# Optimization experiments

Measured on AMD Instinct MI355X. Metric: run time of the kernel, lower is better.

## Reference

```python
import jax, jax.numpy as jnp
import numpy as np

B, N, X, H = 128, 512, 128, 256  # batch, seq len, in features, hidden

_PARAM_SHAPES = [
    ("fg_w_c", (H,)), ("fg_w_h", (H, H)), ("fg_w_x", (H, X)), ("fg_b", (H,)),
    ("ig_w_c", (H,)), ("ig_w_h", (H, H)), ("ig_w_x", (H, X)), ("ig_b", (H,)),
    ("in_w_h", (H, H)), ("in_w_x", (H, X)), ("in_b", (H,)),
    ("og_w_cn", (H,)), ("og_w_h", (H, H)), ("og_w_x", (H, X)), ("og_b", (H,)), ("og_w_t", (H,)),
    ("tg1_w_x", (H, X)), ("tg1_w_t", (H,)), ("tg1_b", (H,)),
    ("tg2_w_x", (H, X)), ("tg2_w_t", (H,)), ("tg2_b", (H,)),
]


def setup_inputs() -> dict:
    key = jax.random.key(0)
    ks = jax.random.split(key, 2 + len(_PARAM_SHAPES))
    stdv = 1.0 / np.sqrt(H)  # torch __init__ re-inits all params uniform(-stdv, stdv)
    inp = {
        "x": jax.random.normal(ks[0], (B, N, X), jnp.float32),
        "t": jax.random.uniform(ks[1], (B, N, 1), jnp.float32),  # time intervals >= 0
    }
    for i, (name, shape) in enumerate(_PARAM_SHAPES):
        inp[name] = jax.random.uniform(ks[2 + i], shape, jnp.float32, -stdv, stdv)
    return inp


def reference(x, t,
              fg_w_c, fg_w_h, fg_w_x, fg_b,
              ig_w_c, ig_w_h, ig_w_x, ig_b,
              in_w_h, in_w_x, in_b,
              og_w_cn, og_w_h, og_w_x, og_b, og_w_t,
              tg1_w_x, tg1_w_t, tg1_b,
              tg2_w_x, tg2_w_t, tg2_b):
    # TimeLSTM_v3 with nn_type = NN_TYPE_LSTM_TIME2.
    # torch stores vector params as [H,1] and x_cur as [B,xm,1]; here squeezed to [H] / [B,xm].
    # Precompute all input-dependent (non-recurrent) gate terms over the whole sequence: [B,N,H]
    fg_x = jnp.einsum('bnx,hx->bnh', x, fg_w_x) + fg_b
    ig_x = jnp.einsum('bnx,hx->bnh', x, ig_w_x) + ig_b
    in_x = jnp.einsum('bnx,hx->bnh', x, in_w_x) + in_b
    og_x = jnp.einsum('bnx,hx->bnh', x, og_w_x) + og_w_t * t + og_b
    # Time gates depend only on x and t -> fully precomputable
    tm1 = jax.nn.sigmoid(jnp.einsum('bnx,hx->bnh', x, tg1_w_x) + jnp.tanh(tg1_w_t * t) + tg1_b)
    tm2 = jax.nn.sigmoid(jnp.einsum('bnx,hx->bnh', x, tg2_w_x) + jnp.tanh(tg2_w_t * t) + tg2_b)

    def step(carry, inputs):
        h, cm = carry  # each [B,H]
        fg_xt, ig_xt, in_xt, og_xt, tm1_t, tm2_t = inputs
        ig = jax.nn.sigmoid(ig_w_c * cm + h @ ig_w_h.T + ig_xt)
        fg = jax.nn.sigmoid(fg_w_c * cm + h @ fg_w_h.T + fg_xt)
        inn = jnp.tanh(h @ in_w_h.T + in_xt)
        cm_hat = fg * cm + ig * tm1_t * inn
        cm_new = fg * cm + ig * tm2_t * inn
        og = jax.nn.sigmoid(og_w_cn * cm_hat + h @ og_w_h.T + og_xt)
        h_new = og * jnp.tanh(cm_hat)
        return (h_new, cm_new), None

    seqs = tuple(jnp.moveaxis(a, 1, 0) for a in (fg_x, ig_x, in_x, og_x, tm1, tm2))  # [N,B,H]
    init = (jnp.zeros((x.shape[0], H), x.dtype), jnp.zeros((x.shape[0], H), x.dtype))
    (h, cm), _ = jax.lax.scan(step, init, seqs)
    return h, cm  # h: [B,H] (torch squeezes trailing 1), cm: [B,H]
```

## Files before the change

### kernel.cpp

```cpp
#include <hip/hip_runtime.h>
#include <math.h>

#define BATCH 128
#define SEQN  512
#define XF    128
#define HF    256
#define BC    16
#define HC    8
#define TCH   8
#define NBLK  256
#define NTHR  256
#define NGRP  8
#define GSZ   32

#define OFF_W    0
#define OFF_WX   8192
#define OFF_G    14336
#define OFF_U    20480
#define OFF_SCR  24576
#define OFF_CM   36864
#define OFF_TV   36992
#define OFF_COEF 37120
#define LDS_WORDS 37216
#define LDS_BYTES (LDS_WORDS * 4)

struct Params {
  const float* x;
  const float* t;
  const float* w_h[4];
  const float* w_x[6];
  const float* coef[12];
  float* h_buf;
  unsigned* flags;
  float* out;
};

__device__ __forceinline__ float sigmoidf_(float v) { return 1.0f / (1.0f + __expf(-v)); }

__device__ __forceinline__ void post_arrive(unsigned* flags, int gi, int mi, unsigned step) {
  __syncthreads();
  if (threadIdx.x == 0) {
    __hip_atomic_store(&flags[(gi * GSZ + mi) * 16], step,
                       __ATOMIC_RELAXED, __HIP_MEMORY_SCOPE_AGENT);
  }
}

__device__ __forceinline__ void wait_peers(unsigned* flags, int gi, int mi, unsigned step) {
  if (threadIdx.x < GSZ && threadIdx.x != (unsigned)mi) {
    const unsigned* f = &flags[(gi * GSZ + threadIdx.x) * 16];
    while (__hip_atomic_load(f, __ATOMIC_RELAXED, __HIP_MEMORY_SCOPE_AGENT) < step) {}
  }
  __syncthreads();
}

__global__ __launch_bounds__(NTHR, 1) void timelstm_kernel(Params p) {
  extern __shared__ float sm[];
  const int tid = threadIdx.x;
  const int bid = blockIdx.x;
  const int gi = bid & 7;
  const int mi = bid >> 3;
  const int b0 = gi * BC;
  const int h0 = mi * HC;

  for (int i = tid; i < 4 * 8 * 256; i += NTHR) {
    int g = i >> 11, j = (i >> 8) & 7, k = i & 255;
    sm[OFF_W + k * 32 + j * 4 + g] = p.w_h[g][(h0 + j) * HF + k];
  }
  for (int i = tid; i < 6 * 8 * 128; i += NTHR) {
    int g = i >> 10, j = (i >> 7) & 7, k = i & 127;
    sm[OFF_WX + k * 48 + j * 6 + g] = p.w_x[g][(h0 + j) * XF + k];
  }
  if (tid < 96) sm[OFF_COEF + tid] = p.coef[tid >> 3][h0 + (tid & 7)];
  if (tid < 128) sm[OFF_CM + tid] = 0.0f;
  if (mi == 0) {
    unsigned long long* hbu = (unsigned long long*)p.h_buf;
    for (int i = tid; i < HF * BC / 2; i += NTHR) {
      const int k = i >> 3;
      __hip_atomic_store(&hbu[k * (BATCH / 2) + b0 / 2 + (i & 7)], 0ull,
                         __ATOMIC_RELAXED, __HIP_MEMORY_SCOPE_AGENT);
    }
  }
  unsigned bstep = 1;
  post_arrive(p.flags, gi, mi, bstep);
  wait_peers(p.flags, gi, mi, bstep);
  ++bstep;

  int cur = 0;
  for (int tc0 = 0; tc0 < SEQN; tc0 += TCH) {
    {
      for (int it = 0; it < BC; ++it) {
        const int b = it, t = (tid >> 5) & 7, k0 = (tid & 31) * 4;
        const float4 v = *(const float4*)&p.x[((size_t)(b0 + b) * SEQN + (tc0 + t)) * XF + k0];
        float vb[4] = {v.x, v.y, v.z, v.w};
#pragma unroll
        for (int u = 0; u < 4; ++u) {
          const int k = k0 + u;
          sm[OFF_U + k * 128 + ((((b) << 3) | t) ^ (((k >> 2) & 7) << 2))] = vb[u];
        }
      }
      if (tid < 128)
        sm[OFF_TV + tid] = p.t[(size_t)(b0 + (tid >> 3)) * SEQN + tc0 + (tid & 7)];
    }
    __syncthreads();
    {
      const int gh = tid >> 7, idx = tid & 127;
      const int j = idx >> 4, b = idx & 15;
      float a0[8], a1[8], a2[8];
#pragma unroll
      for (int u = 0; u < 8; ++u) { a0[u] = 0.f; a1[u] = 0.f; a2[u] = 0.f; }
      const int base = b << 3;
#pragma unroll 2
      for (int k = 0; k < XF; ++k) {
        const int xk = ((k >> 2) & 7) << 2;
        const float4 xlo = *(const float4*)&sm[OFF_U + k * 128 + ((base | 0) ^ xk)];
        const float4 xhi = *(const float4*)&sm[OFF_U + k * 128 + ((base | 4) ^ xk)];
        const float* wr = &sm[OFF_WX + k * 48 + j * 6 + gh * 3];
        const float w0 = wr[0], w1 = wr[1], w2 = wr[2];
        const float xs[8] = {xlo.x, xlo.y, xlo.z, xlo.w, xhi.x, xhi.y, xhi.z, xhi.w};
#pragma unroll
        for (int u = 0; u < 8; ++u) {
          a0[u] += w0 * xs[u];
          a1[u] += w1 * xs[u];
          a2[u] += w2 * xs[u];
        }
      }
      if (gh == 0) {
        const float c0 = sm[OFF_COEF + 0 * 8 + j];
        const float c1 = sm[OFF_COEF + 1 * 8 + j];
        const float c2 = sm[OFF_COEF + 2 * 8 + j];
#pragma unroll
        for (int t = 0; t < 8; ++t) {
          sm[OFF_G + t * 768 + 0 * 128 + idx] = a0[t] + c0;
          sm[OFF_G + t * 768 + 1 * 128 + idx] = a1[t] + c1;
          sm[OFF_G + t * 768 + 2 * 128 + idx] = a2[t] + c2;
        }
      } else {
        const float ogb = sm[OFF_COEF + 3 * 8 + j], ogwt = sm[OFF_COEF + 4 * 8 + j];
        const float t1w = sm[OFF_COEF + 5 * 8 + j], t1b = sm[OFF_COEF + 6 * 8 + j];
        const float t2w = sm[OFF_COEF + 7 * 8 + j], t2b = sm[OFF_COEF + 8 * 8 + j];
#pragma unroll
        for (int t = 0; t < 8; ++t) {
          const float tv = sm[OFF_TV + b * 8 + t];
          sm[OFF_G + t * 768 + 3 * 128 + idx] = a0[t] + ogwt * tv + ogb;
          sm[OFF_G + t * 768 + 4 * 128 + idx] = sigmoidf_(a1[t] + tanhf(t1w * tv) + t1b);
          sm[OFF_G + t * 768 + 5 * 128 + idx] = sigmoidf_(a2[t] + tanhf(t2w * tv) + t2b);
        }
      }
    }
    __syncthreads();

    for (int tt = 0; tt < TCH; ++tt) {
      {
        const unsigned long long* hsrc =
            (const unsigned long long*)(p.h_buf + (size_t)cur * HF * BATCH);
        unsigned long long uv[8];
#pragma unroll
        for (int it = 0; it < 8; ++it) {
          const int i = it * 256 + tid;
          const int k = i >> 3;
          uv[it] = __hip_atomic_load(&hsrc[k * (BATCH / 2) + b0 / 2 + (i & 7)],
                                     __ATOMIC_RELAXED, __HIP_MEMORY_SCOPE_AGENT);
        }
#pragma unroll
        for (int it = 0; it < 8; ++it) {
          const int i = it * 256 + tid;
          union { unsigned long long u; float2 f; } cv;
          cv.u = uv[it];
          *(float2*)&sm[OFF_U + 2 * i] = cv.f;
        }
      }
      __syncthreads();

      const int j = (tid >> 2) & 7, bq = tid & 3, kh = tid >> 5;
      float acc[4][4];
#pragma unroll
      for (int bi = 0; bi < 4; ++bi)
#pragma unroll
        for (int g = 0; g < 4; ++g) acc[bi][g] = 0.f;

      const float* hp = &sm[OFF_U + kh * 512 + bq * 4];
      const float* wp = &sm[OFF_W + kh * 1024 + j * 4];
#pragma unroll 4
      for (int kk = 0; kk < 32; ++kk) {
        const float4 hv = *(const float4*)&hp[kk * 16];
        const float4 wv = *(const float4*)&wp[kk * 32];
        acc[0][0] += hv.x * wv.x; acc[0][1] += hv.x * wv.y; acc[0][2] += hv.x * wv.z; acc[0][3] += hv.x * wv.w;
        acc[1][0] += hv.y * wv.x; acc[1][1] += hv.y * wv.y; acc[1][2] += hv.y * wv.z; acc[1][3] += hv.y * wv.w;
        acc[2][0] += hv.z * wv.x; acc[2][1] += hv.z * wv.y; acc[2][2] += hv.z * wv.z; acc[2][3] += hv.z * wv.w;
        acc[3][0] += hv.w * wv.x; acc[3][1] += hv.w * wv.y; acc[3][2] += hv.w * wv.z; acc[3][3] += hv.w * wv.w;
      }
      {
        const int outb = j * 16 + bq * 4;
#pragma unroll
        for (int g = 0; g < 4; ++g) {
          float4 s = {acc[0][g], acc[1][g], acc[2][g], acc[3][g]};
          *(float4*)&sm[OFF_SCR + kh * 512 + g * 128 + outb] = s;
        }
      }
      __syncthreads();

      if (tid < 128) {
        const int idx = tid, j2 = tid >> 4, bl = tid & 15;
        float pre[4];
#pragma unroll
        for (int g = 0; g < 4; ++g) {
          float s = 0.f;
#pragma unroll
          for (int k2 = 0; k2 < 8; ++k2) s += sm[OFF_SCR + k2 * 512 + g * 128 + idx];
          pre[g] = s;
        }
        const float cm = sm[OFF_CM + idx];
        const float* gt = &sm[OFF_G + tt * 768];
        const float fgx = gt[idx],        igx = gt[128 + idx], inx = gt[256 + idx];
        const float ogx = gt[384 + idx],  tm1 = gt[512 + idx], tm2 = gt[640 + idx];
        const float igv = sigmoidf_(sm[OFF_COEF + 10 * 8 + j2] * cm + pre[1] + igx);
        const float fgv = sigmoidf_(sm[OFF_COEF + 9 * 8 + j2] * cm + pre[0] + fgx);
        const float inn = tanhf(pre[2] + inx);
        const float cbase = fgv * cm, cinn = igv * inn;
        const float cmh = cbase + cinn * tm1;
        const float cmn = cbase + cinn * tm2;
        const float ogv = sigmoidf_(sm[OFF_COEF + 11 * 8 + j2] * cmh + pre[3] + ogx);
        const float hn  = ogv * tanhf(cmh);
        sm[OFF_CM + idx] = cmn;
        const float hn_hi = __shfl_down(hn, 1, 64);
        if ((bl & 1) == 0) {
          union { float2 f; unsigned long long u; } cv;
          cv.f.x = hn; cv.f.y = hn_hi;
          unsigned long long* hdst =
              (unsigned long long*)(p.h_buf + (size_t)(cur ^ 1) * HF * BATCH +
                                    (size_t)(h0 + j2) * BATCH + b0 + bl);
          __hip_atomic_store(hdst, cv.u, __ATOMIC_RELAXED, __HIP_MEMORY_SCOPE_AGENT);
        }
        if (tc0 + tt == SEQN - 1) {
          p.out[(size_t)(b0 + bl) * HF + h0 + j2] = hn;
          p.out[(size_t)BATCH * HF + (size_t)(b0 + bl) * HF + h0 + j2] = cmn;
        }
      }
      post_arrive(p.flags, gi, mi, bstep);
      wait_peers(p.flags, gi, mi, bstep);
      ++bstep;
      cur ^= 1;
    }
  }
}

extern "C" void kernel_launch(void* const* d_in, const int* in_sizes, int n_in,
                              void* d_out, int out_size, void* d_ws, size_t ws_size,
                              hipStream_t stream) {
  (void)in_sizes; (void)n_in; (void)out_size; (void)ws_size;
  Params p;
  p.x = (const float*)d_in[0];
  p.t = (const float*)d_in[1];
  p.w_h[0] = (const float*)d_in[3];
  p.w_h[1] = (const float*)d_in[7];
  p.w_h[2] = (const float*)d_in[10];
  p.w_h[3] = (const float*)d_in[14];
  p.w_x[0] = (const float*)d_in[4];
  p.w_x[1] = (const float*)d_in[8];
  p.w_x[2] = (const float*)d_in[11];
  p.w_x[3] = (const float*)d_in[15];
  p.w_x[4] = (const float*)d_in[18];
  p.w_x[5] = (const float*)d_in[21];
  p.coef[0]  = (const float*)d_in[5];
  p.coef[1]  = (const float*)d_in[9];
  p.coef[2]  = (const float*)d_in[12];
  p.coef[3]  = (const float*)d_in[16];
  p.coef[4]  = (const float*)d_in[17];
  p.coef[5]  = (const float*)d_in[19];
  p.coef[6]  = (const float*)d_in[20];
  p.coef[7]  = (const float*)d_in[22];
  p.coef[8]  = (const float*)d_in[23];
  p.coef[9]  = (const float*)d_in[2];
  p.coef[10] = (const float*)d_in[6];
  p.coef[11] = (const float*)d_in[13];
  p.flags = (unsigned*)d_ws;
  p.h_buf = (float*)((char*)d_ws + 32768);
  p.out = (float*)d_out;

  hipMemsetAsync(d_ws, 0, 16384, stream);
  hipFuncSetAttribute((const void*)timelstm_kernel,
                      hipFuncAttributeMaxDynamicSharedMemorySize, LDS_BYTES);
  timelstm_kernel<<<dim3(NBLK), dim3(NTHR), LDS_BYTES, stream>>>(p);
}
```

Baseline: 2.885 ms.

## Replace LDS split-K reduction with swizzle reduction and single-wave barrier polling

```diff
diff --git a/kernel.cpp b/kernel.cpp
--- a/kernel.cpp
+++ b/kernel.cpp
@@ -16,12 +16,12 @@
 #define OFF_W    0
 #define OFF_WX   8192
 #define OFF_G    14336
-#define OFF_U    20480
-#define OFF_SCR  24576
+#define OFF_X    20480
 #define OFF_CM   36864
 #define OFF_TV   36992
 #define OFF_COEF 37120
-#define LDS_WORDS 37216
+#define OFF_GO   37216
+#define LDS_WORDS 37220
 #define LDS_BYTES (LDS_WORDS * 4)
 
 struct Params {
@@ -37,6 +37,10 @@
 
 __device__ __forceinline__ float sigmoidf_(float v) { return 1.0f / (1.0f + __expf(-v)); }
 
+__device__ __forceinline__ float swzx1(float v) { return __int_as_float(__builtin_amdgcn_ds_swizzle(__float_as_int(v), 0x041F)); }
+__device__ __forceinline__ float swzx2(float v) { return __int_as_float(__builtin_amdgcn_ds_swizzle(__float_as_int(v), 0x081F)); }
+__device__ __forceinline__ float swzx4(float v) { return __int_as_float(__builtin_amdgcn_ds_swizzle(__float_as_int(v), 0x101F)); }
+
 __device__ __forceinline__ void post_arrive(unsigned* flags, int gi, int mi, unsigned step) {
   __syncthreads();
   if (threadIdx.x == 0) {
@@ -45,12 +49,23 @@
   }
 }
 
-__device__ __forceinline__ void wait_peers(unsigned* flags, int gi, int mi, unsigned step) {
-  if (threadIdx.x < GSZ && threadIdx.x != (unsigned)mi) {
-    const unsigned* f = &flags[(gi * GSZ + threadIdx.x) * 16];
-    while (__hip_atomic_load(f, __ATOMIC_RELAXED, __HIP_MEMORY_SCOPE_AGENT) < step) {}
-  }
-  __syncthreads();
+__device__ __forceinline__ void wave_wait(float* sm, const unsigned* flags,
+                                          int gi, int mi, unsigned step) {
+  unsigned* go = (unsigned*)&sm[OFF_GO];
+  const int tid = threadIdx.x;
+  if (tid < 64) {
+    const bool need = (tid < GSZ) && (tid != mi);
+    const unsigned* f = &flags[(gi * GSZ + (tid & (GSZ - 1))) * 16];
+    while (true) {
+      unsigned v = need ? __hip_atomic_load(f, __ATOMIC_RELAXED, __HIP_MEMORY_SCOPE_AGENT)
+                        : step;
+      if (__all((int)(v >= step))) break;
+    }
+    if (tid == 0)
+      __hip_atomic_store(go, step, __ATOMIC_RELAXED, __HIP_MEMORY_SCOPE_WORKGROUP);
+  } else {
+    while (__hip_atomic_load(go, __ATOMIC_RELAXED, __HIP_MEMORY_SCOPE_WORKGROUP) < step) {}
+  }
 }
 
 __global__ __launch_bounds__(NTHR, 1) void timelstm_kernel(Params p) {
@@ -72,6 +87,7 @@
   }
   if (tid < 96) sm[OFF_COEF + tid] = p.coef[tid >> 3][h0 + (tid & 7)];
   if (tid < 128) sm[OFF_CM + tid] = 0.0f;
+  if (tid == 0) *(unsigned*)&sm[OFF_GO] = 0u;
   if (mi == 0) {
     unsigned long long* hbu = (unsigned long long*)p.h_buf;
     for (int i = tid; i < HF * BC / 2; i += NTHR) {
@@ -80,22 +96,33 @@
                          __ATOMIC_RELAXED, __HIP_MEMORY_SCOPE_AGENT);
     }
   }
+  post_arrive(p.flags, gi, mi, 1u);
   unsigned bstep = 1;
-  post_arrive(p.flags, gi, mi, bstep);
-  wait_peers(p.flags, gi, mi, bstep);
-  ++bstep;
-
   int cur = 0;
+
+  const int lane = tid & 63;
+  const int bq = tid >> 6;
+  const int kh = lane & 7;
+  const int j  = lane >> 3;
+
   for (int tc0 = 0; tc0 < SEQN; tc0 += TCH) {
     {
-      for (int it = 0; it < BC; ++it) {
-        const int b = it, t = (tid >> 5) & 7, k0 = (tid & 31) * 4;
-        const float4 v = *(const float4*)&p.x[((size_t)(b0 + b) * SEQN + (tc0 + t)) * XF + k0];
-        float vb[4] = {v.x, v.y, v.z, v.w};
+      float4 xr[16];
+#pragma unroll
+      for (int it = 0; it < 16; ++it) {
+        const int ri = it * 8 + (tid >> 5);
+        const int k0 = (tid & 31) * 4;
+        xr[it] = *(const float4*)&p.x[((size_t)(b0 + (ri >> 3)) * SEQN + (tc0 + (ri & 7))) * XF + k0];
+      }
+#pragma unroll
+      for (int it = 0; it < 16; ++it) {
+        const int ri = it * 8 + (tid >> 5);
+        const int k0 = (tid & 31) * 4;
+        const float xb[4] = {xr[it].x, xr[it].y, xr[it].z, xr[it].w};
 #pragma unroll
         for (int u = 0; u < 4; ++u) {
           const int k = k0 + u;
-          sm[OFF_U + k * 128 + ((((b) << 3) | t) ^ (((k >> 2) & 7) << 2))] = vb[u];
+          sm[OFF_X + k * 128 + (ri ^ (((k >> 2) & 7) << 2))] = xb[u];
         }
       }
       if (tid < 128)
@@ -103,53 +130,48 @@
     }
     __syncthreads();
     {
-      const int gh = tid >> 7, idx = tid & 127;
-      const int j = idx >> 4, b = idx & 15;
-      float a0[8], a1[8], a2[8];
-#pragma unroll
-      for (int u = 0; u < 8; ++u) { a0[u] = 0.f; a1[u] = 0.f; a2[u] = 0.f; }
-      const int base = b << 3;
-#pragma unroll 2
+      const int c = tid >> 3, r = tid & 7;
+      const int c4 = c << 2;
+      float a0[4], a1[4], a2[4], a3[4], a4[4], a5[4];
+#pragma unroll
+      for (int u = 0; u < 4; ++u) { a0[u]=0.f; a1[u]=0.f; a2[u]=0.f; a3[u]=0.f; a4[u]=0.f; a5[u]=0.f; }
+      const float* wxp = &sm[OFF_WX + r * 6];
+#pragma unroll 4
       for (int k = 0; k < XF; ++k) {
-        const int xk = ((k >> 2) & 7) << 2;
-        const float4 xlo = *(const float4*)&sm[OFF_U + k * 128 + ((base | 0) ^ xk)];
-        const float4 xhi = *(const float4*)&sm[OFF_U + k * 128 + ((base | 4) ^ xk)];
-        const float* wr = &sm[OFF_WX + k * 48 + j * 6 + gh * 3];
-        const float w0 = wr[0], w1 = wr[1], w2 = wr[2];
-        const float xs[8] = {xlo.x, xlo.y, xlo.z, xlo.w, xhi.x, xhi.y, xhi.z, xhi.w};
-#pragma unroll
-        for (int u = 0; u < 8; ++u) {
-          a0[u] += w0 * xs[u];
-          a1[u] += w1 * xs[u];
-          a2[u] += w2 * xs[u];
-        }
-      }
-      if (gh == 0) {
-        const float c0 = sm[OFF_COEF + 0 * 8 + j];
-        const float c1 = sm[OFF_COEF + 1 * 8 + j];
-        const float c2 = sm[OFF_COEF + 2 * 8 + j];
-#pragma unroll
-        for (int t = 0; t < 8; ++t) {
-          sm[OFF_G + t * 768 + 0 * 128 + idx] = a0[t] + c0;
-          sm[OFF_G + t * 768 + 1 * 128 + idx] = a1[t] + c1;
-          sm[OFF_G + t * 768 + 2 * 128 + idx] = a2[t] + c2;
-        }
-      } else {
-        const float ogb = sm[OFF_COEF + 3 * 8 + j], ogwt = sm[OFF_COEF + 4 * 8 + j];
-        const float t1w = sm[OFF_COEF + 5 * 8 + j], t1b = sm[OFF_COEF + 6 * 8 + j];
-        const float t2w = sm[OFF_COEF + 7 * 8 + j], t2b = sm[OFF_COEF + 8 * 8 + j];
-#pragma unroll
-        for (int t = 0; t < 8; ++t) {
-          const float tv = sm[OFF_TV + b * 8 + t];
-          sm[OFF_G + t * 768 + 3 * 128 + idx] = a0[t] + ogwt * tv + ogb;
-          sm[OFF_G + t * 768 + 4 * 128 + idx] = sigmoidf_(a1[t] + tanhf(t1w * tv) + t1b);
-          sm[OFF_G + t * 768 + 5 * 128 + idx] = sigmoidf_(a2[t] + tanhf(t2w * tv) + t2b);
-        }
+        const float4 xv = *(const float4*)&sm[OFF_X + k * 128 + (c4 ^ (((k >> 2) & 7) << 2))];
+        const float2 wA = *(const float2*)&wxp[k * 48 + 0];
+        const float2 wB = *(const float2*)&wxp[k * 48 + 2];
+        const float2 wC = *(const float2*)&wxp[k * 48 + 4];
+        const float xs[4] = {xv.x, xv.y, xv.z, xv.w};
+#pragma unroll
+        for (int u = 0; u < 4; ++u) {
+          a0[u] += wA.x * xs[u]; a1[u] += wA.y * xs[u];
+          a2[u] += wB.x * xs[u]; a3[u] += wB.y * xs[u];
+          a4[u] += wC.x * xs[u]; a5[u] += wC.y * xs[u];
+        }
+      }
+      const float cfg  = sm[OFF_COEF + 0 * 8 + r], cig  = sm[OFF_COEF + 1 * 8 + r];
+      const float cin  = sm[OFF_COEF + 2 * 8 + r];
+      const float cogb = sm[OFF_COEF + 3 * 8 + r], cogwt = sm[OFF_COEF + 4 * 8 + r];
+      const float ct1w = sm[OFF_COEF + 5 * 8 + r], ct1b = sm[OFF_COEF + 6 * 8 + r];
+      const float ct2w = sm[OFF_COEF + 7 * 8 + r], ct2b = sm[OFF_COEF + 8 * 8 + r];
+#pragma unroll
+      for (int u = 0; u < 4; ++u) {
+        const int bt = c4 + u, b = bt >> 3, t = bt & 7;
+        const float tv = sm[OFF_TV + bt];
+        float* gp = &sm[OFF_G + t * 768 + b * 8 + r];
+        gp[0]   = a0[u] + cfg;
+        gp[128] = a1[u] + cig;
+        gp[256] = a2[u] + cin;
+        gp[384] = a3[u] + cogwt * tv + cogb;
+        gp[512] = sigmoidf_(a4[u] + tanhf(ct1w * tv) + ct1b);
+        gp[640] = sigmoidf_(a5[u] + tanhf(ct2w * tv) + ct2b);
       }
     }
     __syncthreads();
 
     for (int tt = 0; tt < TCH; ++tt) {
+      wave_wait(sm, p.flags, gi, mi, bstep);
       {
         const unsigned long long* hsrc =
             (const unsigned long long*)(p.h_buf + (size_t)cur * HF * BATCH);
@@ -164,23 +186,23 @@
 #pragma unroll
         for (int it = 0; it < 8; ++it) {
           const int i = it * 256 + tid;
+          const int k = i >> 3, pr = i & 7;
           union { unsigned long long u; float2 f; } cv;
           cv.u = uv[it];
-          *(float2*)&sm[OFF_U + 2 * i] = cv.f;
+          *(float2*)&sm[OFF_X + k * 16 + ((pr * 2) ^ (((k >> 5) & 3) << 2))] = cv.f;
         }
       }
       __syncthreads();
 
-      const int j = (tid >> 2) & 7, bq = tid & 3, kh = tid >> 5;
       float acc[4][4];
 #pragma unroll
       for (int bi = 0; bi < 4; ++bi)
 #pragma unroll
         for (int g = 0; g < 4; ++g) acc[bi][g] = 0.f;
 
-      const float* hp = &sm[OFF_U + kh * 512 + bq * 4];
-      const float* wp = &sm[OFF_W + kh * 1024 + j * 4];
-#pragma unroll 4
+      const float* hp = &sm[OFF_X + kh * 512 + ((bq ^ (kh & 3)) << 2)];
+      const float* wp = &sm[OFF_W + kh * 1024 + (j << 2)];
+#pragma unroll 8
       for (int kk = 0; kk < 32; ++kk) {
         const float4 hv = *(const float4*)&hp[kk * 16];
         const float4 wv = *(const float4*)&wp[kk * 32];
@@ -189,55 +211,62 @@
         acc[2][0] += hv.z * wv.x; acc[2][1] += hv.z * wv.y; acc[2][2] += hv.z * wv.z; acc[2][3] += hv.z * wv.w;
         acc[3][0] += hv.w * wv.x; acc[3][1] += hv.w * wv.y; acc[3][2] += hv.w * wv.z; acc[3][3] += hv.w * wv.w;
       }
+
+      const int kb0 = kh & 1, kb1 = (kh >> 1) & 1;
+      float s1[2][4];
+#pragma unroll
+      for (int pp = 0; pp < 2; ++pp)
+#pragma unroll
+        for (int g = 0; g < 4; ++g) {
+          const float mine  = kb0 ? acc[2 * pp + 1][g] : acc[2 * pp][g];
+          const float yours = kb0 ? acc[2 * pp][g]     : acc[2 * pp + 1][g];
+          s1[pp][g] = mine + swzx1(yours);
+        }
+      float s2[4];
+#pragma unroll
+      for (int g = 0; g < 4; ++g) {
+        const float mine  = kb1 ? s1[1][g] : s1[0][g];
+        const float yours = kb1 ? s1[0][g] : s1[1][g];
+        s2[g] = mine + swzx2(yours);
+      }
+      float pre[4];
+#pragma unroll
+      for (int g = 0; g < 4; ++g) pre[g] = s2[g] + swzx4(s2[g]);
+
       {
-        const int outb = j * 16 + bq * 4;
-#pragma unroll
-        for (int g = 0; g < 4; ++g) {
-          float4 s = {acc[0][g], acc[1][g], acc[2][g], acc[3][g]};
-          *(float4*)&sm[OFF_SCR + kh * 512 + g * 128 + outb] = s;
-        }
-      }
-      __syncthreads();
-
-      if (tid < 128) {
-        const int idx = tid, j2 = tid >> 4, bl = tid & 15;
-        float pre[4];
-#pragma unroll
-        for (int g = 0; g < 4; ++g) {
-          float s = 0.f;
-#pragma unroll
-          for (int k2 = 0; k2 < 8; ++k2) s += sm[OFF_SCR + k2 * 512 + g * 128 + idx];
-          pre[g] = s;
-        }
-        const float cm = sm[OFF_CM + idx];
-        const float* gt = &sm[OFF_G + tt * 768];
-        const float fgx = gt[idx],        igx = gt[128 + idx], inx = gt[256 + idx];
-        const float ogx = gt[384 + idx],  tm1 = gt[512 + idx], tm2 = gt[640 + idx];
-        const float igv = sigmoidf_(sm[OFF_COEF + 10 * 8 + j2] * cm + pre[1] + igx);
-        const float fgv = sigmoidf_(sm[OFF_COEF + 9 * 8 + j2] * cm + pre[0] + fgx);
+        const int bi = kh & 3;
+        const int b  = (bq << 2) + bi;
+        const int ib = b * 8 + j;
+        const float cm = sm[OFF_CM + ib];
+        const float* gt = &sm[OFF_G + tt * 768 + ib];
+        const float fgx = gt[0],   igx = gt[128], inx = gt[256];
+        const float ogx = gt[384], tm1 = gt[512], tm2 = gt[640];
+        const float igv = sigmoidf_(sm[OFF_COEF + 10 * 8 + j] * cm + pre[1] + igx);
+        const float fgv = sigmoidf_(sm[OFF_COEF + 9 * 8 + j] * cm + pre[0] + fgx);
         const float inn = tanhf(pre[2] + inx);
         const float cbase = fgv * cm, cinn = igv * inn;
         const float cmh = cbase + cinn * tm1;
         const float cmn = cbase + cinn * tm2;
-        const float ogv = sigmoidf_(sm[OFF_COEF + 11 * 8 + j2] * cmh + pre[3] + ogx);
+        const float ogv = sigmoidf_(sm[OFF_COEF + 11 * 8 + j] * cmh + pre[3] + ogx);
         const float hn  = ogv * tanhf(cmh);
-        sm[OFF_CM + idx] = cmn;
-        const float hn_hi = __shfl_down(hn, 1, 64);
-        if ((bl & 1) == 0) {
-          union { float2 f; unsigned long long u; } cv;
-          cv.f.x = hn; cv.f.y = hn_hi;
-          unsigned long long* hdst =
-              (unsigned long long*)(p.h_buf + (size_t)(cur ^ 1) * HF * BATCH +
-                                    (size_t)(h0 + j2) * BATCH + b0 + bl);
-          __hip_atomic_store(hdst, cv.u, __ATOMIC_RELAXED, __HIP_MEMORY_SCOPE_AGENT);
-        }
-        if (tc0 + tt == SEQN - 1) {
-          p.out[(size_t)(b0 + bl) * HF + h0 + j2] = hn;
-          p.out[(size_t)BATCH * HF + (size_t)(b0 + bl) * HF + h0 + j2] = cmn;
-        }
-      }
-      post_arrive(p.flags, gi, mi, bstep);
-      wait_peers(p.flags, gi, mi, bstep);
+        const float hn2 = swzx1(hn);
+        if (kh < 4) {
+          sm[OFF_CM + ib] = cmn;
+          if (!(kh & 1)) {
+            union { float2 f; unsigned long long u; } cv;
+            cv.f.x = hn; cv.f.y = hn2;
+            unsigned long long* hdst =
+                (unsigned long long*)(p.h_buf + (size_t)(cur ^ 1) * HF * BATCH +
+                                      (size_t)(h0 + j) * BATCH + b0 + b);
+            __hip_atomic_store(hdst, cv.u, __ATOMIC_RELAXED, __HIP_MEMORY_SCOPE_AGENT);
+          }
+          if (tc0 + tt == SEQN - 1) {
+            p.out[(size_t)(b0 + b) * HF + h0 + j] = hn;
+            p.out[(size_t)BATCH * HF + (size_t)(b0 + b) * HF + h0 + j] = cmn;
+          }
+        }
+      }
+      post_arrive(p.flags, gi, mi, bstep + 1);
       ++bstep;
       cur ^= 1;
     }
```

Result: faster. 2.727 ms (-5.5%).
